# Optimization experiments

Measured on AMD Instinct MI355X. Metric: run time of the kernel, lower is better.

## Reference

```python
import jax, jax.numpy as jnp
import numpy as np

B, N, D_IN, D_H, D_OUT = 16384, 16, 256, 128, 32


def setup_inputs() -> dict:
    key = jax.random.key(0)
    ks = jax.random.split(key, 6)
    batch_graph = jax.random.normal(ks[0], (B, N, D_IN), dtype=jnp.float32)
    adj = jax.random.uniform(ks[1], (B, N, N), dtype=jnp.float32)
    # xavier_normal with gain=0.02 as in reset_parameters_xavier
    def xavier(k, fan_in, fan_out):
        std = 0.02 * np.sqrt(2.0 / (fan_in + fan_out))
        return jax.random.normal(k, (fan_in, fan_out), dtype=jnp.float32) * std
    W1 = xavier(ks[2], D_IN, D_H)
    W2 = xavier(ks[3], D_H, D_H // 2)
    W3 = xavier(ks[4], D_H // 2, D_OUT)
    b1 = jnp.zeros((D_H,), jnp.float32)
    b2 = jnp.zeros((D_H // 2,), jnp.float32)
    b3 = jnp.zeros((D_OUT,), jnp.float32)
    return {"batch_graph": batch_graph, "adj": adj,
            "W1": W1, "b1": b1, "W2": W2, "b2": b2, "W3": W3, "b3": b3}


def _gcn_layer(x, adj, W, b):
    # support = x @ W  (node-wise dense); output = adj @ support (per-graph aggregation)
    support = jnp.einsum('bnd,df->bnf', x, W)
    return jnp.einsum('bnm,bmf->bnf', adj, support) + b


def reference(batch_graph, adj, W1, b1, W2, b2, W3, b3):
    # The torch code builds a (B*N, B*N) block-diagonal adjacency and runs
    # mm + spmm; mathematically identical to batched per-graph matmuls.
    # Dropout is identity in eval mode.
    x = jax.nn.relu(_gcn_layer(batch_graph, adj, W1, b1))
    x = jax.nn.relu(_gcn_layer(x, adj, W2, b2))
    big_output = _gcn_layer(x, adj, W3, b3)          # [B, N, 32]
    # repeat(1, 16//N, 1) then mean over dim 1: repeating copies does not
    # change the mean, so this equals mean over the node dim.
    out = jnp.mean(big_output, axis=1, keepdims=True)  # [B, 1, 32]
    out = jnp.transpose(out, (0, 2, 1)).reshape(out.shape[0], 32, 1, 1)
    return out
```

## Files before the change

kernel.cpp:

```cpp
#include <hip/hip_runtime.h>


typedef _Float16 half4_t __attribute__((ext_vector_type(4)));
typedef _Float16 half8_t __attribute__((ext_vector_type(8)));
typedef float    float4_t __attribute__((ext_vector_type(4)));

__global__ __launch_bounds__(256) void pack_weights(
    const float* __restrict__ W1, const float* __restrict__ W2,
    const float* __restrict__ W3, _Float16* __restrict__ wf)
{
    const int idx = blockIdx.x * 256 + threadIdx.x;
    if (idx < 4096) {
        const int lane = idx & 63, ks = (idx >> 6) & 7, nt = idx >> 9;
        const int k0 = ks * 32 + ((lane >> 4) << 3), n = nt * 16 + (lane & 15);
        half8_t h;
        #pragma unroll
        for (int j = 0; j < 8; ++j) h[j] = (_Float16)W1[(k0 + j) * 128 + n];
        *(half8_t*)(wf + (size_t)idx * 8) = h;
    } else if (idx < 5120) {
        const int i = idx - 4096;
        const int lane = i & 63, ks = (i >> 6) & 3, nt = i >> 8;
        const int k0 = ks * 32 + ((lane >> 4) << 3), n = nt * 16 + (lane & 15);
        half8_t h;
        #pragma unroll
        for (int j = 0; j < 8; ++j) h[j] = (_Float16)W2[(k0 + j) * 64 + n];
        *(half8_t*)(wf + 32768 + (size_t)i * 8) = h;
    } else if (idx < 5376) {
        const int i = idx - 5120;
        const int lane = i & 63, ks = (i >> 6) & 1, nt = i >> 7;
        const int k0 = ks * 32 + ((lane >> 4) << 3), n = nt * 16 + (lane & 15);
        half8_t h;
        #pragma unroll
        for (int j = 0; j < 8; ++j) h[j] = (_Float16)W3[(k0 + j) * 32 + n];
        *(half8_t*)(wf + 40960 + (size_t)i * 8) = h;
    }
}

__global__ __launch_bounds__(256) void gcn_mfma(
    const float* __restrict__ x,
    const float* __restrict__ adj,
    const float* __restrict__ b1, const float* __restrict__ b2,
    const float* __restrict__ b3,
    const _Float16* __restrict__ wf,
    float* __restrict__ out)
{
    constexpr int XW = 264;
    constexpr int A1W = 136;
    constexpr int A2W = 72;
    constexpr int PW = 16 * XW + 16 * A1W + 256 + 16;
    __shared__ _Float16 smem[4 * PW];

    const int t = threadIdx.x;
    const int lane = t & 63;
    const int w = t >> 6;
    const int g = blockIdx.x * 4 + w;
    const int q = lane >> 4, n16 = lane & 15;

    _Float16* sx   = smem + w * PW;
    _Float16* sa1  = sx + 16 * XW;
    _Float16* sadj = sa1 + 16 * A1W;
    _Float16* sc   = sadj + 256;
    _Float16* sa2  = sx;

    {
        const float* xg = x + (size_t)g * 4096;
        #pragma unroll
        for (int i = 0; i < 16; ++i) {
            float4_t v = *(const float4_t*)(xg + i * 256 + lane * 4);
            half4_t h;
            h[0] = (_Float16)v[0]; h[1] = (_Float16)v[1];
            h[2] = (_Float16)v[2]; h[3] = (_Float16)v[3];
            *(half4_t*)(sx + i * XW + lane * 4) = h;
        }
    }
    {
        const float* ag = adj + (size_t)g * 256;
        float4_t v = *(const float4_t*)(ag + lane * 4);
        half4_t h;
        h[0] = (_Float16)v[0]; h[1] = (_Float16)v[1];
        h[2] = (_Float16)v[2]; h[3] = (_Float16)v[3];
        *(half4_t*)(sadj + (lane >> 2) * 16 + (lane & 3) * 4) = h;
        float4_t s = v;
        #pragma unroll
        for (int d = 4; d < 64; d <<= 1) {
            s[0] += __shfl_xor(s[0], d);
            s[1] += __shfl_xor(s[1], d);
            s[2] += __shfl_xor(s[2], d);
            s[3] += __shfl_xor(s[3], d);
        }
        if (lane < 4) {
            half4_t hc;
            hc[0] = (_Float16)(s[0] * 0.0625f); hc[1] = (_Float16)(s[1] * 0.0625f);
            hc[2] = (_Float16)(s[2] * 0.0625f); hc[3] = (_Float16)(s[3] * 0.0625f);
            *(half4_t*)(sc + lane * 4) = hc;
        }
    }

    const half4_t adjA = *(const half4_t*)(sadj + n16 * 16 + q * 4);
    const float4_t zero = {0.f, 0.f, 0.f, 0.f};

    float4_t acc1[8];
    #pragma unroll
    for (int nt = 0; nt < 8; ++nt) acc1[nt] = zero;
    for (int ks = 0; ks < 8; ++ks) {
        half8_t a = *(const half8_t*)(sx + n16 * XW + ks * 32 + q * 8);
        #pragma unroll
        for (int nt = 0; nt < 8; ++nt) {
            half8_t b = *(const half8_t*)(wf + ((size_t)(nt * 8 + ks) * 64 + lane) * 8);
            acc1[nt] = __builtin_amdgcn_mfma_f32_16x16x32_f16(a, b, acc1[nt], 0, 0, 0);
        }
    }
    #pragma unroll
    for (int nt = 0; nt < 8; ++nt) {
        half4_t p;
        p[0] = (_Float16)acc1[nt][0]; p[1] = (_Float16)acc1[nt][1];
        p[2] = (_Float16)acc1[nt][2]; p[3] = (_Float16)acc1[nt][3];
        float4_t m = __builtin_amdgcn_mfma_f32_16x16x16f16(adjA, p, zero, 0, 0, 0);
        const float bias = b1[nt * 16 + n16];
        #pragma unroll
        for (int r = 0; r < 4; ++r)
            sa1[(q * 4 + r) * A1W + nt * 16 + n16] = (_Float16)fmaxf(m[r] + bias, 0.f);
    }

    float4_t acc2[4];
    #pragma unroll
    for (int nt = 0; nt < 4; ++nt) acc2[nt] = zero;
    for (int ks = 0; ks < 4; ++ks) {
        half8_t a = *(const half8_t*)(sa1 + n16 * A1W + ks * 32 + q * 8);
        #pragma unroll
        for (int nt = 0; nt < 4; ++nt) {
            half8_t b = *(const half8_t*)(wf + 32768 + ((size_t)(nt * 4 + ks) * 64 + lane) * 8);
            acc2[nt] = __builtin_amdgcn_mfma_f32_16x16x32_f16(a, b, acc2[nt], 0, 0, 0);
        }
    }
    #pragma unroll
    for (int nt = 0; nt < 4; ++nt) {
        half4_t p;
        p[0] = (_Float16)acc2[nt][0]; p[1] = (_Float16)acc2[nt][1];
        p[2] = (_Float16)acc2[nt][2]; p[3] = (_Float16)acc2[nt][3];
        float4_t m = __builtin_amdgcn_mfma_f32_16x16x16f16(adjA, p, zero, 0, 0, 0);
        const float bias = b2[nt * 16 + n16];
        #pragma unroll
        for (int r = 0; r < 4; ++r)
            sa2[(q * 4 + r) * A2W + nt * 16 + n16] = (_Float16)fmaxf(m[r] + bias, 0.f);
    }

    float4_t acc3[2];
    acc3[0] = zero; acc3[1] = zero;
    for (int ks = 0; ks < 2; ++ks) {
        half8_t a = *(const half8_t*)(sa2 + n16 * A2W + ks * 32 + q * 8);
        #pragma unroll
        for (int nt = 0; nt < 2; ++nt) {
            half8_t b = *(const half8_t*)(wf + 40960 + ((size_t)(nt * 2 + ks) * 64 + lane) * 8);
            acc3[nt] = __builtin_amdgcn_mfma_f32_16x16x32_f16(a, b, acc3[nt], 0, 0, 0);
        }
    }
    const half4_t cf = *(const half4_t*)(sc + q * 4);
    #pragma unroll
    for (int nt = 0; nt < 2; ++nt) {
        half4_t p;
        p[0] = (_Float16)acc3[nt][0]; p[1] = (_Float16)acc3[nt][1];
        p[2] = (_Float16)acc3[nt][2]; p[3] = (_Float16)acc3[nt][3];
        float4_t o = __builtin_amdgcn_mfma_f32_16x16x16f16(cf, p, zero, 0, 0, 0);
        if (q == 0)
            out[(size_t)g * 32 + nt * 16 + n16] = o[0] + b3[nt * 16 + n16];
    }
}

extern "C" void kernel_launch(void* const* d_in, const int* in_sizes, int n_in,
                              void* d_out, int out_size, void* d_ws, size_t ws_size,
                              hipStream_t stream) {
    const float* x   = (const float*)d_in[0];
    const float* adj = (const float*)d_in[1];
    const float* W1  = (const float*)d_in[2];
    const float* b1  = (const float*)d_in[3];
    const float* W2  = (const float*)d_in[4];
    const float* b2  = (const float*)d_in[5];
    const float* W3  = (const float*)d_in[6];
    const float* b3  = (const float*)d_in[7];
    _Float16* wf = (_Float16*)d_ws;
    pack_weights<<<21, 256, 0, stream>>>(W1, W2, W3, wf);
    gcn_mfma<<<4096, 256, 0, stream>>>(x, adj, b1, b2, b3, wf, (float*)d_out);
}
```

Baseline: 393.6 us.

## Load x straight into MFMA A-fragments and emit transposed vectorized activations

Stops staging the per-graph x tile in shared memory. Each lane now reads its fp32 A-fragment directly from global memory and converts it to half in registers, which shrinks LDS use and adds a launch_bounds occupancy hint of 4. The aggregation MFMA swaps its operands so the result comes out transposed, which lets bias loads and activation stores be vectorized as half4 writes to LDS. The risk is that the direct global reads are strided 32-byte chunks per lane instead of fully coalesced rows, and their latency is no longer hidden behind an LDS prefetch.

Result: slower. 405.9 us (+3.1%).

```diff
diff --git a/kernel.cpp b/kernel.cpp
--- a/kernel.cpp
+++ b/kernel.cpp
@@ -36,7 +36,7 @@
     }
 }
 
-__global__ __launch_bounds__(256) void gcn_mfma(
+__global__ __launch_bounds__(256, 4) void gcn_mfma(
     const float* __restrict__ x,
     const float* __restrict__ adj,
     const float* __restrict__ b1, const float* __restrict__ b2,
@@ -44,10 +44,9 @@
     const _Float16* __restrict__ wf,
     float* __restrict__ out)
 {
-    constexpr int XW = 264;
     constexpr int A1W = 136;
     constexpr int A2W = 72;
-    constexpr int PW = 16 * XW + 16 * A1W + 256 + 16;
+    constexpr int PW = 16 * A1W + 16 * A2W + 256 + 16;
     __shared__ _Float16 smem[4 * PW];
 
     const int t = threadIdx.x;
@@ -56,23 +55,11 @@
     const int g = blockIdx.x * 4 + w;
     const int q = lane >> 4, n16 = lane & 15;
 
-    _Float16* sx   = smem + w * PW;
-    _Float16* sa1  = sx + 16 * XW;
-    _Float16* sadj = sa1 + 16 * A1W;
+    _Float16* sa1  = smem + w * PW;
+    _Float16* sa2  = sa1 + 16 * A1W;
+    _Float16* sadj = sa1 + 16 * A1W + 16 * A2W;
     _Float16* sc   = sadj + 256;
-    _Float16* sa2  = sx;
 
-    {
-        const float* xg = x + (size_t)g * 4096;
-        #pragma unroll
-        for (int i = 0; i < 16; ++i) {
-            float4_t v = *(const float4_t*)(xg + i * 256 + lane * 4);
-            half4_t h;
-            h[0] = (_Float16)v[0]; h[1] = (_Float16)v[1];
-            h[2] = (_Float16)v[2]; h[3] = (_Float16)v[3];
-            *(half4_t*)(sx + i * XW + lane * 4) = h;
-        }
-    }
     {
         const float* ag = adj + (size_t)g * 256;
         float4_t v = *(const float4_t*)(ag + lane * 4);
@@ -96,18 +83,28 @@
         }
     }
 
-    const half4_t adjA = *(const half4_t*)(sadj + n16 * 16 + q * 4);
+    const half4_t adjF = *(const half4_t*)(sadj + n16 * 16 + q * 4);
     const float4_t zero = {0.f, 0.f, 0.f, 0.f};
 
     float4_t acc1[8];
     #pragma unroll
     for (int nt = 0; nt < 8; ++nt) acc1[nt] = zero;
-    for (int ks = 0; ks < 8; ++ks) {
-        half8_t a = *(const half8_t*)(sx + n16 * XW + ks * 32 + q * 8);
+    {
+        const float* xr = x + (size_t)g * 4096 + n16 * 256 + q * 8;
         #pragma unroll
-        for (int nt = 0; nt < 8; ++nt) {
-            half8_t b = *(const half8_t*)(wf + ((size_t)(nt * 8 + ks) * 64 + lane) * 8);
-            acc1[nt] = __builtin_amdgcn_mfma_f32_16x16x32_f16(a, b, acc1[nt], 0, 0, 0);
+        for (int ks = 0; ks < 8; ++ks) {
+            float4_t v0 = *(const float4_t*)(xr + ks * 32);
+            float4_t v1 = *(const float4_t*)(xr + ks * 32 + 4);
+            half8_t a;
+            a[0] = (_Float16)v0[0]; a[1] = (_Float16)v0[1];
+            a[2] = (_Float16)v0[2]; a[3] = (_Float16)v0[3];
+            a[4] = (_Float16)v1[0]; a[5] = (_Float16)v1[1];
+            a[6] = (_Float16)v1[2]; a[7] = (_Float16)v1[3];
+            #pragma unroll
+            for (int nt = 0; nt < 8; ++nt) {
+                half8_t b = *(const half8_t*)(wf + ((size_t)(nt * 8 + ks) * 64 + lane) * 8);
+                acc1[nt] = __builtin_amdgcn_mfma_f32_16x16x32_f16(a, b, acc1[nt], 0, 0, 0);
+            }
         }
     }
     #pragma unroll
@@ -115,11 +112,12 @@
         half4_t p;
         p[0] = (_Float16)acc1[nt][0]; p[1] = (_Float16)acc1[nt][1];
         p[2] = (_Float16)acc1[nt][2]; p[3] = (_Float16)acc1[nt][3];
-        float4_t m = __builtin_amdgcn_mfma_f32_16x16x16f16(adjA, p, zero, 0, 0, 0);
-        const float bias = b1[nt * 16 + n16];
+        float4_t m = __builtin_amdgcn_mfma_f32_16x16x16f16(p, adjF, zero, 0, 0, 0);
+        float4_t bias = *(const float4_t*)(b1 + nt * 16 + q * 4);
+        half4_t hm;
         #pragma unroll
-        for (int r = 0; r < 4; ++r)
-            sa1[(q * 4 + r) * A1W + nt * 16 + n16] = (_Float16)fmaxf(m[r] + bias, 0.f);
+        for (int r = 0; r < 4; ++r) hm[r] = (_Float16)fmaxf(m[r] + bias[r], 0.f);
+        *(half4_t*)(sa1 + n16 * A1W + nt * 16 + q * 4) = hm;
     }
 
     float4_t acc2[4];
@@ -138,11 +136,12 @@
         half4_t p;
         p[0] = (_Float16)acc2[nt][0]; p[1] = (_Float16)acc2[nt][1];
         p[2] = (_Float16)acc2[nt][2]; p[3] = (_Float16)acc2[nt][3];
-        float4_t m = __builtin_amdgcn_mfma_f32_16x16x16f16(adjA, p, zero, 0, 0, 0);
-        const float bias = b2[nt * 16 + n16];
+        float4_t m = __builtin_amdgcn_mfma_f32_16x16x16f16(p, adjF, zero, 0, 0, 0);
+        float4_t bias = *(const float4_t*)(b2 + nt * 16 + q * 4);
+        half4_t hm;
         #pragma unroll
-        for (int r = 0; r < 4; ++r)
-            sa2[(q * 4 + r) * A2W + nt * 16 + n16] = (_Float16)fmaxf(m[r] + bias, 0.f);
+        for (int r = 0; r < 4; ++r) hm[r] = (_Float16)fmaxf(m[r] + bias[r], 0.f);
+        *(half4_t*)(sa2 + n16 * A2W + nt * 16 + q * 4) = hm;
     }
 
     float4_t acc3[2];
```
